# Kernel tuning notes

Hardware: AMD Instinct MI355X
Metric: run time of the kernel (lower is better)

## Reference

```python
import jax, jax.numpy as jnp
import numpy as np

NUM_C = 1000
B, L = 8, 1024
D, H, NB, DFF = 512, 8, 4, 2048
DK = D // H
EPS = 1e-5


def _ln(x, s, b):
    mu = jnp.mean(x, axis=-1, keepdims=True)
    var = jnp.mean((x - mu) ** 2, axis=-1, keepdims=True)
    return (x - mu) * jax.lax.rsqrt(var + EPS) * s + b


def setup_inputs() -> dict:
    key = jax.random.key(0)
    ks = iter(jax.random.split(key, 64))

    def nrm(shape, scale=0.02):
        return jax.random.normal(next(ks), shape, dtype=jnp.float32) * scale

    inp = {
        "q": jax.random.randint(next(ks), (B, L), 0, NUM_C),
        "r": jax.random.randint(next(ks), (B, L), 0, 2),
        # embeddings
        "ctx_emb": nrm((NUM_C * 2, D)),
        "val_emb": nrm((NUM_C * 2, D)),
        "skill_emb": nrm((NUM_C, D)),
        "pos_emb": nrm((L, D)),
        # attention projections, stacked over blocks
        "Wq": nrm((NB, D, D)), "bq": jnp.zeros((NB, D)),
        "Wk": nrm((NB, D, D)), "bk": jnp.zeros((NB, D)),
        "Wv": nrm((NB, D, D)), "bv": jnp.zeros((NB, D)),
        "Wo": nrm((NB, D, D)), "bo": jnp.zeros((NB, D)),
        # layer norms (ctx / val streams, pre- and post-FFN)
        "ln1c_s": jnp.ones((NB, D)), "ln1c_b": jnp.zeros((NB, D)),
        "ln1v_s": jnp.ones((NB, D)), "ln1v_b": jnp.zeros((NB, D)),
        "ln2c_s": jnp.ones((NB, D)), "ln2c_b": jnp.zeros((NB, D)),
        "ln2v_s": jnp.ones((NB, D)), "ln2v_b": jnp.zeros((NB, D)),
        # FFNs
        "fc1c_W": nrm((NB, D, DFF)), "fc1c_b": jnp.zeros((NB, DFF)),
        "fc2c_W": nrm((NB, DFF, D)), "fc2c_b": jnp.zeros((NB, D)),
        "fc1v_W": nrm((NB, D, DFF)), "fc1v_b": jnp.zeros((NB, DFF)),
        "fc2v_W": nrm((NB, DFF, D)), "fc2v_b": jnp.zeros((NB, D)),
        # prediction head: [3D -> DFF -> 256 -> 1]
        "hW1": nrm((3 * D, DFF)), "hb1": jnp.zeros((DFF,)),
        "hW2": nrm((DFF, 256)), "hb2": jnp.zeros((256,)),
        "hW3": nrm((256, 1)), "hb3": jnp.zeros((1,)),
    }
    return inp


def reference(q, r, ctx_emb, val_emb, skill_emb, pos_emb,
              Wq, bq, Wk, bk, Wv, bv, Wo, bo,
              ln1c_s, ln1c_b, ln1v_s, ln1v_b,
              ln2c_s, ln2c_b, ln2v_s, ln2v_b,
              fc1c_W, fc1c_b, fc2c_W, fc2c_b,
              fc1v_W, fc1v_b, fc2v_W, fc2v_b,
              hW1, hb1, hW2, hb2, hW3, hb3):
    inter = q + NUM_C * r                       # [B, L] interaction ids
    pos = pos_emb[None, :L, :]
    ctx = ctx_emb[inter] + pos                  # [B, L, D]
    val = val_emb[inter] + pos                  # [B, L, D]
    causal = jnp.tril(jnp.ones((L, L), dtype=bool))
    scale = 1.0 / (DK ** 0.5)

    for i in range(NB):
        # dual-stream MHA: Q,K from ctx; V from val
        Q = (ctx @ Wq[i] + bq[i]).reshape(B, L, H, DK)
        K = (ctx @ Wk[i] + bk[i]).reshape(B, L, H, DK)
        V = (val @ Wv[i] + bv[i]).reshape(B, L, H, DK)
        # fp32 scores (as in torch source), mask==0 -> -inf, softmax
        scores = jnp.einsum('bqhd,bkhd->bhqk', Q.astype(jnp.float32),
                            K.astype(jnp.float32)) * scale
        scores = jnp.where(causal, scores, -jnp.inf)
        attn = jax.nn.softmax(scores, axis=-1)  # dropout = identity (eval)
        out = jnp.einsum('bhqk,bkhd->bqhd', attn, V).reshape(B, L, D)
        out = out @ Wo[i] + bo[i]
        # shared attn output added to both streams, separate norms
        ctx = _ln(ctx + out, ln1c_s[i], ln1c_b[i])
        val = _ln(val + out, ln1v_s[i], ln1v_b[i])
        # dual FFNs
        f_ctx = jax.nn.relu(ctx @ fc1c_W[i] + fc1c_b[i]) @ fc2c_W[i] + fc2c_b[i]
        ctx = _ln(ctx + f_ctx, ln2c_s[i], ln2c_b[i])
        f_val = jax.nn.relu(val @ fc1v_W[i] + fc1v_b[i]) @ fc2v_W[i] + fc2v_b[i]
        val = _ln(val + f_val, ln2v_s[i], ln2v_b[i])

    feat = jnp.concatenate([ctx, val, skill_emb[q]], axis=-1)  # [B, L, 3D]
    h = jax.nn.relu(feat @ hW1 + hb1)
    h = jax.nn.relu(h @ hW2 + hb2)
    logits = (h @ hW3 + hb3)[..., 0]
    return jax.nn.sigmoid(logits)               # [B, L] p(correct)
```

## Files before the change

### kernel.cpp

```cpp
#include <hip/hip_runtime.h>
#include <hip/hip_bf16.h>
#include <math.h>

#define TOK 8192
#define DM 512
#define NH 8
#define DKH 64
#define DFFN 2048
#define SEQ 1024
#define NBLK 4
#define NUMC 1000

typedef __attribute__((ext_vector_type(8))) short bf16x8;
typedef __attribute__((ext_vector_type(4))) float f32x4;
typedef __attribute__((ext_vector_type(4))) ushort u16x4;
typedef __hip_bfloat16 bf16;

__device__ __forceinline__ void gload_lds16(const ushort* g, ushort* l) {
    __builtin_amdgcn_global_load_lds(
        (const __attribute__((address_space(1))) void*)g,
        (__attribute__((address_space(3))) void*)l, 16, 0, 0);
}

__global__ __launch_bounds__(256) void embed_kernel(
    const int* __restrict__ q, const int* __restrict__ r,
    const float* __restrict__ ctx_emb, const float* __restrict__ val_emb,
    const float* __restrict__ pos_emb,
    float* __restrict__ ctx32, float* __restrict__ val32,
    bf16* __restrict__ ctx16, bf16* __restrict__ val16)
{
    const int t = blockIdx.x;
    const int inter = q[t] + NUMC * r[t];
    const int l = t & (SEQ - 1);
    const float* ce = ctx_emb + (size_t)inter * DM;
    const float* ve = val_emb + (size_t)inter * DM;
    const float* pe = pos_emb + (size_t)l * DM;
    const size_t o = (size_t)t * DM;
    for (int d = threadIdx.x; d < DM; d += 256) {
        float p = pe[d];
        float c = ce[d] + p;
        float v = ve[d] + p;
        ctx32[o + d] = c; val32[o + d] = v;
        ctx16[o + d] = __float2bfloat16(c);
        val16[o + d] = __float2bfloat16(v);
    }
}

__global__ __launch_bounds__(256) void transpose_kernel(
    const float* __restrict__ src, bf16* __restrict__ dst,
    int K, int N, long sb, long db)
{
    __shared__ float t[32][33];
    src += (long)blockIdx.z * sb;
    dst += (long)blockIdx.z * db;
    const int n0 = blockIdx.x * 32;
    const int k0 = blockIdx.y * 32;
    const int tx = threadIdx.x;
    const int ty = threadIdx.y;
    for (int i = ty; i < 32; i += 8) t[i][tx] = src[(size_t)(k0 + i) * N + n0 + tx];
    __syncthreads();
    for (int i = ty; i < 32; i += 8)
        dst[(size_t)(n0 + i) * K + k0 + tx] = __float2bfloat16(t[tx][i]);
}

template<int BN, bool OUTBF16>
__global__ __launch_bounds__(256, 3) void mfma_gemm(
    const ushort* __restrict__ A, const ushort* __restrict__ Bt,
    const float* __restrict__ bias1, const float* __restrict__ bias2, int split,
    void* __restrict__ Cv, int N, int K, int relu, int vtmode,
    const ushort* __restrict__ A1, const ushort* __restrict__ Bt1,
    const float* __restrict__ bias1_1, void* __restrict__ Cv1)
{
    if (blockIdx.z) { A = A1; Bt = Bt1; bias1 = bias1_1; Cv = Cv1; }
    constexpr int MI = (BN == 128) ? 4 : 2;
    constexpr int BR = BN / 32;
    __shared__ ushort As[128 * 64];
    __shared__ ushort Bs[BN * 64];
    const int tid = threadIdx.x;
    const int wave = tid >> 6;
    const int lane = tid & 63;
    const int ln = lane & 15;
    const int kq = lane >> 4;
    const int nx = gridDim.x;
    const int lin = blockIdx.x + nx * blockIdx.y;
    const int loc = lin >> 3;
    const int mdiv = loc / nx;
    const int bm = ((lin & 7) + 8 * mdiv) * 128;
    const int bn = (loc - mdiv * nx) * BN;
    const int wr = (BN == 128) ? (wave >> 1) * 64 : wave * 32;
    const int wc = (BN == 128) ? (wave & 1) * 64 : 0;

    const int trow = tid >> 3;
    const int gcb = (tid & 7) ^ (trow & 7);
    const ushort* Ab = A + (size_t)(bm + trow) * K + gcb * 8;
    const ushort* Bb = Bt + (size_t)(bn + trow) * K + gcb * 8;
    ushort* AsW = As + wave * 512;
    ushort* BsW = Bs + wave * 512;

    f32x4 acc[MI][4];
#pragma unroll
    for (int i = 0; i < MI; ++i)
#pragma unroll
        for (int j = 0; j < 4; ++j) acc[i][j] = (f32x4){0.f, 0.f, 0.f, 0.f};

    for (int k0 = 0; k0 < K; k0 += 64) {
        __syncthreads();
#pragma unroll
        for (int p = 0; p < 4; ++p)
            gload_lds16(Ab + (size_t)32 * p * K + k0, AsW + p * 2048);
#pragma unroll
        for (int p = 0; p < BR; ++p)
            gload_lds16(Bb + (size_t)32 * p * K + k0, BsW + p * 2048);
        __syncthreads();
#pragma unroll
        for (int half = 0; half < 2; ++half) {
            const int cb = ((half * 4 + kq) ^ (ln & 7)) * 8;
            bf16x8 bfr[4];
#pragma unroll
            for (int j = 0; j < 4; ++j)
                bfr[j] = *(const bf16x8*)&Bs[(wc + j * 16 + ln) * 64 + cb];
#pragma unroll
            for (int i = 0; i < MI; ++i) {
                const bf16x8 af = *(const bf16x8*)&As[(wr + i * 16 + ln) * 64 + cb];
#pragma unroll
                for (int j = 0; j < 4; ++j)
                    acc[i][j] = __builtin_amdgcn_mfma_f32_16x16x32_bf16(af, bfr[j], acc[i][j], 0, 0, 0);
            }
        }
    }

#pragma unroll
    for (int i = 0; i < MI; ++i) {
        const int rowb = bm + wr + i * 16 + kq * 4;
#pragma unroll
        for (int j = 0; j < 4; ++j) {
            const int colg = bn + wc + j * 16 + ln;
            const float bv = (colg < split) ? bias1[colg] : bias2[colg - split];
            if (vtmode) {
                union { u16x4 v; ushort u[4]; } pk;
#pragma unroll
                for (int rr = 0; rr < 4; ++rr) {
                    float v = acc[i][j][rr] + bv;
                    bf16 t = __float2bfloat16(v);
                    pk.u[rr] = *(ushort*)&t;
                }
                *(u16x4*)((ushort*)Cv + ((size_t)(rowb >> 10) * 512 + colg) * 1024 + (rowb & 1023)) = pk.v;
            } else {
#pragma unroll
                for (int rr = 0; rr < 4; ++rr) {
                    float v = acc[i][j][rr] + bv;
                    if (relu) v = fmaxf(v, 0.f);
                    if (OUTBF16)
                        ((bf16*)Cv)[(size_t)(rowb + rr) * N + colg] = __float2bfloat16(v);
                    else
                        ((float*)Cv)[(size_t)(rowb + rr) * N + colg] = v;
                }
            }
        }
    }
}

__global__ __launch_bounds__(256) void attn_kernel(
    const bf16* __restrict__ QK, const bf16* __restrict__ Vt,
    bf16* __restrict__ Og)
{
    __shared__ ushort Qs[64 * 64];
    __shared__ ushort Ks[64 * 64];
    __shared__ ushort Vs[64 * 64];
    __shared__ ushort Ps[4 * 16 * 68];

    const int tid = threadIdx.x;
    const int wave = tid >> 6, lane = tid & 63;
    const int ln = lane & 15, kq = lane >> 4;
    const int lin = blockIdx.x + 16 * blockIdx.y;
    const int loc = lin >> 3;
    const int qt = loc & 15;
    const int bh = (lin & 7) + 8 * (loc >> 4);
    const int b = bh >> 3, h = bh & 7;

    const int srow = tid >> 3;
    const int sgcb = (tid & 7) ^ (srow & 7);
    const ushort* gQ = (const ushort*)QK + (size_t)(b * SEQ + qt * 64 + srow) * 1024 + h * 64 + sgcb * 8;
    const ushort* gK = (const ushort*)QK + (size_t)(b * SEQ + srow) * 1024 + 512 + h * 64 + sgcb * 8;
    const ushort* gV = (const ushort*)Vt + (size_t)(bh * 64 + srow) * 1024 + sgcb * 8;
    ushort* QsW = Qs + wave * 512;
    ushort* KsW = Ks + wave * 512;
    ushort* VsW = Vs + wave * 512;

    gload_lds16(gQ, QsW);
    gload_lds16(gQ + 32 * 1024, QsW + 2048);

    float rs[4];
    f32x4 oacc[4];
#pragma unroll
    for (int r = 0; r < 4; ++r) { rs[r] = 0.f; oacc[r] = (f32x4){0.f, 0.f, 0.f, 0.f}; }
    const float sc2 = 0.125f * 1.4426950408889634f;

    const int cb0 = (kq ^ (ln & 7)) * 8;
    const int cb1 = ((4 + kq) ^ (ln & 7)) * 8;

    for (int kt = 0; kt <= qt; ++kt) {
        __syncthreads();
        gload_lds16(gK + (size_t)kt * 64 * 1024, KsW);
        gload_lds16(gK + (size_t)(kt * 64 + 32) * 1024, KsW + 2048);
        gload_lds16(gV + kt * 64, VsW);
        gload_lds16(gV + 32 * 1024 + kt * 64, VsW + 2048);
        __syncthreads();

        const bf16x8 aq0 = *(const bf16x8*)&Qs[(wave * 16 + ln) * 64 + cb0];
        const bf16x8 aq1 = *(const bf16x8*)&Qs[(wave * 16 + ln) * 64 + cb1];
        f32x4 s[4];
#pragma unroll
        for (int c = 0; c < 4; ++c) {
            const bf16x8 bk0 = *(const bf16x8*)&Ks[(c * 16 + ln) * 64 + cb0];
            const bf16x8 bk1 = *(const bf16x8*)&Ks[(c * 16 + ln) * 64 + cb1];
            s[c] = (f32x4){0.f, 0.f, 0.f, 0.f};
            s[c] = __builtin_amdgcn_mfma_f32_16x16x32_bf16(aq0, bk0, s[c], 0, 0, 0);
            s[c] = __builtin_amdgcn_mfma_f32_16x16x32_bf16(aq1, bk1, s[c], 0, 0, 0);
        }
        if (kt == qt) {
#pragma unroll
            for (int c = 0; c < 4; ++c)
#pragma unroll
                for (int r = 0; r < 4; ++r) {
                    const int qg = wave * 16 + kq * 4 + r;
                    const int jg = c * 16 + ln;
                    const float pv = (jg <= qg) ? exp2f(s[c][r] * sc2) : 0.f;
                    rs[r] += pv;
                    *(bf16*)&Ps[wave * 1088 + (kq * 4 + r) * 68 + c * 16 + ln] = __float2bfloat16(pv);
                }
        } else {
#pragma unroll
            for (int c = 0; c < 4; ++c)
#pragma unroll
                for (int r = 0; r < 4; ++r) {
                    const float pv = exp2f(s[c][r] * sc2);
                    rs[r] += pv;
                    *(bf16*)&Ps[wave * 1088 + (kq * 4 + r) * 68 + c * 16 + ln] = __float2bfloat16(pv);
                }
        }
        const bf16x8 ap0 = *(const bf16x8*)&Ps[wave * 1088 + ln * 68 + kq * 8];
        const bf16x8 ap1 = *(const bf16x8*)&Ps[wave * 1088 + ln * 68 + 32 + kq * 8];
#pragma unroll
        for (int c2 = 0; c2 < 4; ++c2) {
            const bf16x8 bv0 = *(const bf16x8*)&Vs[(c2 * 16 + ln) * 64 + cb0];
            const bf16x8 bv1 = *(const bf16x8*)&Vs[(c2 * 16 + ln) * 64 + cb1];
            oacc[c2] = __builtin_amdgcn_mfma_f32_16x16x32_bf16(ap0, bv0, oacc[c2], 0, 0, 0);
            oacc[c2] = __builtin_amdgcn_mfma_f32_16x16x32_bf16(ap1, bv1, oacc[c2], 0, 0, 0);
        }
    }
    float inv[4];
#pragma unroll
    for (int r = 0; r < 4; ++r) {
        float v = rs[r];
        v += __shfl_xor(v, 1);
        v += __shfl_xor(v, 2);
        v += __shfl_xor(v, 4);
        v += __shfl_xor(v, 8);
        inv[r] = 1.f / v;
    }
#pragma unroll
    for (int c2 = 0; c2 < 4; ++c2)
#pragma unroll
        for (int r = 0; r < 4; ++r)
            Og[(size_t)(b * SEQ + qt * 64 + wave * 16 + kq * 4 + r) * 512 + h * 64 + c2 * 16 + ln]
                = __float2bfloat16(oacc[c2][r] * inv[r]);
}

__global__ __launch_bounds__(256) void lnp_kernel(
    const float* __restrict__ x0, const bf16* __restrict__ r0, const float* __restrict__ s0,
    const float* __restrict__ b0, float* __restrict__ of0, bf16* __restrict__ oh0,
    const float* __restrict__ x1, const bf16* __restrict__ r1, const float* __restrict__ s1,
    const float* __restrict__ b1, float* __restrict__ of1, bf16* __restrict__ oh1)
{
    const float* x = x0; const bf16* res = r0; const float* s = s0; const float* bb = b0;
    float* of = of0; bf16* oh = oh0;
    if (blockIdx.y) { x = x1; res = r1; s = s1; bb = b1; of = of1; oh = oh1; }
    __shared__ float w1[4], w2[4];
    const size_t o = (size_t)blockIdx.x * DM;
    const int i0 = threadIdx.x, i1 = threadIdx.x + 256;
    const float v0 = x[o + i0] + __bfloat162float(res[o + i0]);
    const float v1 = x[o + i1] + __bfloat162float(res[o + i1]);
    float sum = v0 + v1;
#pragma unroll
    for (int off = 32; off; off >>= 1) sum += __shfl_down(sum, off);
    if ((threadIdx.x & 63) == 0) w1[threadIdx.x >> 6] = sum;
    __syncthreads();
    const float mu = (w1[0] + w1[1] + w1[2] + w1[3]) * (1.f / DM);
    const float d0 = v0 - mu, d1 = v1 - mu;
    float vs = d0 * d0 + d1 * d1;
#pragma unroll
    for (int off = 32; off; off >>= 1) vs += __shfl_down(vs, off);
    if ((threadIdx.x & 63) == 0) w2[threadIdx.x >> 6] = vs;
    __syncthreads();
    const float rstd = rsqrtf((w2[0] + w2[1] + w2[2] + w2[3]) * (1.f / DM) + 1e-5f);
    const float o0 = d0 * rstd * s[i0] + bb[i0];
    const float o1 = d1 * rstd * s[i1] + bb[i1];
    of[o + i0] = o0; of[o + i1] = o1;
    oh[o + i0] = __float2bfloat16(o0);
    oh[o + i1] = __float2bfloat16(o1);
}

__global__ __launch_bounds__(256) void gather_kernel(
    const bf16* __restrict__ ctx16, const bf16* __restrict__ val16,
    const float* __restrict__ skill, const int* __restrict__ q,
    bf16* __restrict__ feat)
{
    const int t = blockIdx.x;
    const float* sp = skill + (size_t)q[t] * DM;
    const bf16* cp = ctx16 + (size_t)t * DM;
    const bf16* vp = val16 + (size_t)t * DM;
    bf16* fp = feat + (size_t)t * (3 * DM);
    for (int d = threadIdx.x; d < DM; d += 256) {
        fp[d] = cp[d];
        fp[DM + d] = vp[d];
        fp[2 * DM + d] = __float2bfloat16(sp[d]);
    }
}

__global__ __launch_bounds__(256) void logits_kernel(
    const float* __restrict__ h2, const float* __restrict__ w,
    const float* __restrict__ bptr, float* __restrict__ out)
{
    __shared__ float w1[4];
    const int t = blockIdx.x;
    float sum = h2[(size_t)t * 256 + threadIdx.x] * w[threadIdx.x];
#pragma unroll
    for (int off = 32; off; off >>= 1) sum += __shfl_down(sum, off);
    if ((threadIdx.x & 63) == 0) w1[threadIdx.x >> 6] = sum;
    __syncthreads();
    if (threadIdx.x == 0) {
        const float logit = w1[0] + w1[1] + w1[2] + w1[3] + bptr[0];
        out[t] = 1.f / (1.f + __expf(-logit));
    }
}

extern "C" void kernel_launch(void* const* d_in, const int* in_sizes, int n_in,
                              void* d_out, int out_size, void* d_ws, size_t ws_size,
                              hipStream_t stream)
{
    const int*   q         = (const int*)d_in[0];
    const int*   r         = (const int*)d_in[1];
    const float* ctx_emb   = (const float*)d_in[2];
    const float* val_emb   = (const float*)d_in[3];
    const float* skill_emb = (const float*)d_in[4];
    const float* pos_emb   = (const float*)d_in[5];
    const float* Wq = (const float*)d_in[6];
    const float* bq = (const float*)d_in[7];
    const float* Wk = (const float*)d_in[8];
    const float* bk = (const float*)d_in[9];
    const float* Wv = (const float*)d_in[10];
    const float* bv = (const float*)d_in[11];
    const float* Wo = (const float*)d_in[12];
    const float* bo = (const float*)d_in[13];
    const float* ln1c_s = (const float*)d_in[14];
    const float* ln1c_b = (const float*)d_in[15];
    const float* ln1v_s = (const float*)d_in[16];
    const float* ln1v_b = (const float*)d_in[17];
    const float* ln2c_s = (const float*)d_in[18];
    const float* ln2c_b = (const float*)d_in[19];
    const float* ln2v_s = (const float*)d_in[20];
    const float* ln2v_b = (const float*)d_in[21];
    const float* fc1c_W = (const float*)d_in[22];
    const float* fc1c_b = (const float*)d_in[23];
    const float* fc2c_W = (const float*)d_in[24];
    const float* fc2c_b = (const float*)d_in[25];
    const float* fc1v_W = (const float*)d_in[26];
    const float* fc1v_b = (const float*)d_in[27];
    const float* fc2v_W = (const float*)d_in[28];
    const float* fc2v_b = (const float*)d_in[29];
    const float* hW1 = (const float*)d_in[30];
    const float* hb1 = (const float*)d_in[31];
    const float* hW2 = (const float*)d_in[32];
    const float* hb2 = (const float*)d_in[33];
    const float* hW3 = (const float*)d_in[34];
    const float* hb3 = (const float*)d_in[35];
    float* out = (float*)d_out;

    char* p = (char*)d_ws;
    auto alloc = [&](size_t bytes) { char* ret = p; p += bytes; return ret; };
    float* ctx32 = (float*)alloc(16777216);
    float* val32 = (float*)alloc(16777216);
    bf16*  ob16c = (bf16*)alloc(8388608);
    bf16*  ob16v = (bf16*)alloc(8388608);
    bf16*  ctx16 = (bf16*)alloc(8388608);
    bf16*  val16 = (bf16*)alloc(8388608);
    bf16*  qk16  = (bf16*)alloc(16777216);
    bf16*  v16pad= (bf16*)alloc(8388608);
    bf16*  vt16  = (bf16*)alloc(8388608);
    bf16*  att16 = (bf16*)alloc(8388608);
    bf16*  mid16c = (bf16*)alloc(33554432);
    bf16*  qkT   = (bf16*)alloc(4194304);
    bf16*  vT    = (bf16*)alloc(2097152);
    bf16*  oT    = (bf16*)alloc(2097152);
    bf16*  fc1cT = (bf16*)alloc(8388608);
    bf16*  fc2cT = (bf16*)alloc(8388608);
    bf16*  fc1vT = (bf16*)alloc(8388608);
    bf16*  fc2vT = (bf16*)alloc(8388608);
    bf16*  hW1T  = (bf16*)alloc(6291456);
    bf16*  hW2T  = (bf16*)alloc(1048576);
    (void)v16pad;
    bf16*  mid16v = qk16;
    bf16*  feat16 = qk16;
    float* h2     = (float*)vt16;

    const dim3 tb(32, 8);
    transpose_kernel<<<dim3(16, 16, 4), tb, 0, stream>>>(Wq, qkT,          512, 512, 262144, 524288);
    transpose_kernel<<<dim3(16, 16, 4), tb, 0, stream>>>(Wk, qkT + 262144, 512, 512, 262144, 524288);
    transpose_kernel<<<dim3(16, 16, 4), tb, 0, stream>>>(Wv, vT, 512, 512, 262144, 262144);
    transpose_kernel<<<dim3(16, 16, 4), tb, 0, stream>>>(Wo, oT, 512, 512, 262144, 262144);
    transpose_kernel<<<dim3(64, 16, 4), tb, 0, stream>>>(fc1c_W, fc1cT, 512, 2048, 1048576, 1048576);
    transpose_kernel<<<dim3(16, 64, 4), tb, 0, stream>>>(fc2c_W, fc2cT, 2048, 512, 1048576, 1048576);
    transpose_kernel<<<dim3(64, 16, 4), tb, 0, stream>>>(fc1v_W, fc1vT, 512, 2048, 1048576, 1048576);
    transpose_kernel<<<dim3(16, 64, 4), tb, 0, stream>>>(fc2v_W, fc2vT, 2048, 512, 1048576, 1048576);
    transpose_kernel<<<dim3(64, 48, 1), tb, 0, stream>>>(hW1, hW1T, 1536, 2048, 0, 0);
    transpose_kernel<<<dim3(8, 64, 1),  tb, 0, stream>>>(hW2, hW2T, 2048, 256, 0, 0);

    embed_kernel<<<TOK, 256, 0, stream>>>(q, r, ctx_emb, val_emb, pos_emb,
                                          ctx32, val32, ctx16, val16);

    for (int i = 0; i < NBLK; ++i) {
        mfma_gemm<128, true><<<dim3(8, 64), 256, 0, stream>>>(
            (const ushort*)ctx16, (const ushort*)(qkT + (size_t)i * 524288),
            bq + i * DM, bk + i * DM, 512, qk16, 1024, 512, 0, 0,
            nullptr, nullptr, nullptr, nullptr);
        mfma_gemm<64, true><<<dim3(8, 64), 256, 0, stream>>>(
            (const ushort*)val16, (const ushort*)(vT + (size_t)i * 262144),
            bv + i * DM, nullptr, 1 << 30, vt16, 512, 512, 0, 1,
            nullptr, nullptr, nullptr, nullptr);
        attn_kernel<<<dim3(16, 64), 256, 0, stream>>>(qk16, vt16, att16);
        mfma_gemm<64, true><<<dim3(8, 64), 256, 0, stream>>>(
            (const ushort*)att16, (const ushort*)(oT + (size_t)i * 262144),
            bo + i * DM, nullptr, 1 << 30, ob16c, 512, 512, 0, 0,
            nullptr, nullptr, nullptr, nullptr);
        lnp_kernel<<<dim3(TOK, 2), 256, 0, stream>>>(
            ctx32, ob16c, ln1c_s + i * DM, ln1c_b + i * DM, ctx32, ctx16,
            val32, ob16c, ln1v_s + i * DM, ln1v_b + i * DM, val32, val16);
        mfma_gemm<128, true><<<dim3(16, 64, 2), 256, 0, stream>>>(
            (const ushort*)ctx16, (const ushort*)(fc1cT + (size_t)i * 1048576),
            fc1c_b + i * DFFN, nullptr, 1 << 30, mid16c, 2048, 512, 1, 0,
            (const ushort*)val16, (const ushort*)(fc1vT + (size_t)i * 1048576),
            fc1v_b + i * DFFN, mid16v);
        mfma_gemm<128, true><<<dim3(4, 64, 2), 256, 0, stream>>>(
            (const ushort*)mid16c, (const ushort*)(fc2cT + (size_t)i * 1048576),
            fc2c_b + i * DM, nullptr, 1 << 30, ob16c, 512, 2048, 0, 0,
            (const ushort*)mid16v, (const ushort*)(fc2vT + (size_t)i * 1048576),
            fc2v_b + i * DM, ob16v);
        lnp_kernel<<<dim3(TOK, 2), 256, 0, stream>>>(
            ctx32, ob16c, ln2c_s + i * DM, ln2c_b + i * DM, ctx32, ctx16,
            val32, ob16v, ln2v_s + i * DM, ln2v_b + i * DM, val32, val16);
    }

    gather_kernel<<<TOK, 256, 0, stream>>>(ctx16, val16, skill_emb, q, feat16);
    mfma_gemm<128, true><<<dim3(16, 64), 256, 0, stream>>>(
        (const ushort*)feat16, (const ushort*)hW1T, hb1, nullptr, 1 << 30, mid16c, 2048, 1536, 1, 0,
        nullptr, nullptr, nullptr, nullptr);
    mfma_gemm<64, false><<<dim3(4, 64), 256, 0, stream>>>(
        (const ushort*)mid16c, (const ushort*)hW2T, hb2, nullptr, 1 << 30, h2, 256, 2048, 1, 0,
        nullptr, nullptr, nullptr, nullptr);
    logits_kernel<<<TOK, 256, 0, stream>>>(h2, hW3, hb3, out);
}
```

Before: 1.133 ms.

## Drop fp32 residual stream, vectorize layernorm, retune GEMM tiles and occupancy

Removes the fp32 ctx/val residual copies so the residual stream is kept only in bf16, cutting the memory traffic of the embedding and layernorm kernels. The layernorm is rewritten to do one row per wave with 8-wide vector loads and shuffle-only reductions, with no shared memory or barriers. GEMM launch bounds are raised to 5 blocks per SM, and the QK and FC2 GEMMs switch to 64-wide N tiles with more blocks. Keeping the residual in bf16 loses precision across the residual chain, and the higher occupancy target may force register spills.

New measurement: 1.271 ms. 12.1% more time.

```diff
diff --git a/kernel.cpp b/kernel.cpp
--- a/kernel.cpp
+++ b/kernel.cpp
@@ -22,11 +22,14 @@
         (__attribute__((address_space(3))) void*)l, 16, 0, 0);
 }
 
+__device__ __forceinline__ float bf2f(ushort u) {
+    union { unsigned int i; float f; } c; c.i = ((unsigned int)u) << 16; return c.f;
+}
+
 __global__ __launch_bounds__(256) void embed_kernel(
     const int* __restrict__ q, const int* __restrict__ r,
     const float* __restrict__ ctx_emb, const float* __restrict__ val_emb,
     const float* __restrict__ pos_emb,
-    float* __restrict__ ctx32, float* __restrict__ val32,
     bf16* __restrict__ ctx16, bf16* __restrict__ val16)
 {
     const int t = blockIdx.x;
@@ -38,11 +41,8 @@
     const size_t o = (size_t)t * DM;
     for (int d = threadIdx.x; d < DM; d += 256) {
         float p = pe[d];
-        float c = ce[d] + p;
-        float v = ve[d] + p;
-        ctx32[o + d] = c; val32[o + d] = v;
-        ctx16[o + d] = __float2bfloat16(c);
-        val16[o + d] = __float2bfloat16(v);
+        ctx16[o + d] = __float2bfloat16(ce[d] + p);
+        val16[o + d] = __float2bfloat16(ve[d] + p);
     }
 }
 
@@ -64,7 +64,7 @@
 }
 
 template<int BN, bool OUTBF16>
-__global__ __launch_bounds__(256, 3) void mfma_gemm(
+__global__ __launch_bounds__(256, 5) void mfma_gemm(
     const ushort* __restrict__ A, const ushort* __restrict__ Bt,
     const float* __restrict__ bias1, const float* __restrict__ bias2, int split,
     void* __restrict__ Cv, int N, int K, int relu, int vtmode,
@@ -268,37 +268,47 @@
 }
 
 __global__ __launch_bounds__(256) void lnp_kernel(
-    const float* __restrict__ x0, const bf16* __restrict__ r0, const float* __restrict__ s0,
-    const float* __restrict__ b0, float* __restrict__ of0, bf16* __restrict__ oh0,
-    const float* __restrict__ x1, const bf16* __restrict__ r1, const float* __restrict__ s1,
-    const float* __restrict__ b1, float* __restrict__ of1, bf16* __restrict__ oh1)
-{
-    const float* x = x0; const bf16* res = r0; const float* s = s0; const float* bb = b0;
-    float* of = of0; bf16* oh = oh0;
-    if (blockIdx.y) { x = x1; res = r1; s = s1; bb = b1; of = of1; oh = oh1; }
-    __shared__ float w1[4], w2[4];
-    const size_t o = (size_t)blockIdx.x * DM;
-    const int i0 = threadIdx.x, i1 = threadIdx.x + 256;
-    const float v0 = x[o + i0] + __bfloat162float(res[o + i0]);
-    const float v1 = x[o + i1] + __bfloat162float(res[o + i1]);
-    float sum = v0 + v1;
-#pragma unroll
-    for (int off = 32; off; off >>= 1) sum += __shfl_down(sum, off);
-    if ((threadIdx.x & 63) == 0) w1[threadIdx.x >> 6] = sum;
-    __syncthreads();
-    const float mu = (w1[0] + w1[1] + w1[2] + w1[3]) * (1.f / DM);
-    const float d0 = v0 - mu, d1 = v1 - mu;
-    float vs = d0 * d0 + d1 * d1;
-#pragma unroll
-    for (int off = 32; off; off >>= 1) vs += __shfl_down(vs, off);
-    if ((threadIdx.x & 63) == 0) w2[threadIdx.x >> 6] = vs;
-    __syncthreads();
-    const float rstd = rsqrtf((w2[0] + w2[1] + w2[2] + w2[3]) * (1.f / DM) + 1e-5f);
-    const float o0 = d0 * rstd * s[i0] + bb[i0];
-    const float o1 = d1 * rstd * s[i1] + bb[i1];
-    of[o + i0] = o0; of[o + i1] = o1;
-    oh[o + i0] = __float2bfloat16(o0);
-    oh[o + i1] = __float2bfloat16(o1);
+    const bf16* __restrict__ x0, const bf16* __restrict__ r0, const float* __restrict__ s0,
+    const float* __restrict__ b0, bf16* __restrict__ o0,
+    const bf16* __restrict__ x1, const bf16* __restrict__ r1, const float* __restrict__ s1,
+    const float* __restrict__ b1, bf16* __restrict__ o1)
+{
+    const bf16* x = x0; const bf16* res = r0; const float* s = s0; const float* bb = b0; bf16* oh = o0;
+    if (blockIdx.y) { x = x1; res = r1; s = s1; bb = b1; oh = o1; }
+    const int wave = threadIdx.x >> 6, lane = threadIdx.x & 63;
+    const size_t row = (size_t)blockIdx.x * 4 + wave;
+    const size_t o = row * DM + lane * 8;
+    const bf16x8 xv = *(const bf16x8*)(x + o);
+    const bf16x8 rv = *(const bf16x8*)(res + o);
+    float v[8];
+    float sum = 0.f;
+#pragma unroll
+    for (int j = 0; j < 8; ++j) {
+        v[j] = bf2f(((const ushort*)&xv)[j]) + bf2f(((const ushort*)&rv)[j]);
+        sum += v[j];
+    }
+#pragma unroll
+    for (int off = 32; off; off >>= 1) sum += __shfl_xor(sum, off);
+    const float mu = sum * (1.f / DM);
+    float vs = 0.f;
+#pragma unroll
+    for (int j = 0; j < 8; ++j) { v[j] -= mu; vs += v[j] * v[j]; }
+#pragma unroll
+    for (int off = 32; off; off >>= 1) vs += __shfl_xor(vs, off);
+    const float rstd = rsqrtf(vs * (1.f / DM) + 1e-5f);
+    const f32x4 sa = *(const f32x4*)(s + lane * 8);
+    const f32x4 sb2 = *(const f32x4*)(s + lane * 8 + 4);
+    const f32x4 ba = *(const f32x4*)(bb + lane * 8);
+    const f32x4 bb2 = *(const f32x4*)(bb + lane * 8 + 4);
+    union { bf16x8 v8; ushort u[8]; } pk;
+#pragma unroll
+    for (int j = 0; j < 4; ++j) {
+        bf16 t0 = __float2bfloat16(v[j] * rstd * sa[j] + ba[j]);
+        bf16 t1 = __float2bfloat16(v[4 + j] * rstd * sb2[j] + bb2[j]);
+        pk.u[j] = *(ushort*)&t0;
+        pk.u[4 + j] = *(ushort*)&t1;
+    }
+    *(bf16x8*)(oh + o) = pk.v8;
 }
 
 __global__ __launch_bounds__(256) void gather_kernel(
@@ -379,8 +389,6 @@
 
     char* p = (char*)d_ws;
     auto alloc = [&](size_t bytes) { char* ret = p; p += bytes; return ret; };
-    float* ctx32 = (float*)alloc(16777216);
-    float* val32 = (float*)alloc(16777216);
     bf16*  ob16c = (bf16*)alloc(8388608);
     bf16*  ob16v = (bf16*)alloc(8388608);
     bf16*  ctx16 = (bf16*)alloc(8388608);
@@ -416,11 +424,10 @@
     transpose_kernel<<<dim3(64, 48, 1), tb, 0, stream>>>(hW1, hW1T, 1536, 2048, 0, 0);
     transpose_kernel<<<dim3(8, 64, 1),  tb, 0, stream>>>(hW2, hW2T, 2048, 256, 0, 0);
 
-    embed_kernel<<<TOK, 256, 0, stream>>>(q, r, ctx_emb, val_emb, pos_emb,
-                                          ctx32, val32, ctx16, val16);
+    embed_kernel<<<TOK, 256, 0, stream>>>(q, r, ctx_emb, val_emb, pos_emb, ctx16, val16);
 
     for (int i = 0; i < NBLK; ++i) {
-        mfma_gemm<128, true><<<dim3(8, 64), 256, 0, stream>>>(
+        mfma_gemm<64, true><<<dim3(16, 64), 256, 0, stream>>>(
             (const ushort*)ctx16, (const ushort*)(qkT + (size_t)i * 524288),
             bq + i * DM, bk + i * DM, 512, qk16, 1024, 512, 0, 0,
             nullptr, nullptr, nullptr, nullptr);
@@ -433,22 +440,22 @@
             (const ushort*)att16, (const ushort*)(oT + (size_t)i * 262144),
             bo + i * DM, nullptr, 1 << 30, ob16c, 512, 512, 0, 0,
             nullptr, nullptr, nullptr, nullptr);
-        lnp_kernel<<<dim3(TOK, 2), 256, 0, stream>>>(
-            ctx32, ob16c, ln1c_s + i * DM, ln1c_b + i * DM, ctx32, ctx16,
-            val32, ob16c, ln1v_s + i * DM, ln1v_b + i * DM, val32, val16);
+        lnp_kernel<<<dim3(TOK / 4, 2), 256, 0, stream>>>(
+            ctx16, ob16c, ln1c_s + i * DM, ln1c_b + i * DM, ctx16,
+            val16, ob16c, ln1v_s + i * DM, ln1v_b + i * DM, val16);
         mfma_gemm<128, true><<<dim3(16, 64, 2), 256, 0, stream>>>(
             (const ushort*)ctx16, (const ushort*)(fc1cT + (size_t)i * 1048576),
             fc1c_b + i * DFFN, nullptr, 1 << 30, mid16c, 2048, 512, 1, 0,
             (const ushort*)val16, (const ushort*)(fc1vT + (size_t)i * 1048576),
             fc1v_b + i * DFFN, mid16v);
-        mfma_gemm<128, true><<<dim3(4, 64, 2), 256, 0, stream>>>(
+        mfma_gemm<64, true><<<dim3(8, 64, 2), 256, 0, stream>>>(
             (const ushort*)mid16c, (const ushort*)(fc2cT + (size_t)i * 1048576),
             fc2c_b + i * DM, nullptr, 1 << 30, ob16c, 512, 2048, 0, 0,
             (const ushort*)mid16v, (const ushort*)(fc2vT + (size_t)i * 1048576),
             fc2v_b + i * DM, ob16v);
-        lnp_kernel<<<dim3(TOK, 2), 256, 0, stream>>>(
-            ctx32, ob16c, ln2c_s + i * DM, ln2c_b + i * DM, ctx32, ctx16,
-            val32, ob16v, ln2v_s + i * DM, ln2v_b + i * DM, val32, val16);
+        lnp_kernel<<<dim3(TOK / 4, 2), 256, 0, stream>>>(
+            ctx16, ob16c, ln2c_s + i * DM, ln2c_b + i * DM, ctx16,
+            val16, ob16v, ln2v_s + i * DM, ln2v_b + i * DM, val16);
     }
 
     gather_kernel<<<TOK, 256, 0, stream>>>(ctx16, val16, skill_emb, q, feat16);
```
